# Kernel tuning notes

Measured on AMD Instinct MI355X. Metric: run time of the kernel, lower is better.

## Reference

```python
import jax, jax.numpy as jnp
import numpy as np
from jax import lax

N, L, E, ED, H = 100000, 48, 1600000, 17, 48

def _lin_init(k, fan_in, fan_out):
    kw, kb = jax.random.split(k)
    s = 1.0 / np.sqrt(fan_in)
    W = jax.random.uniform(kw, (fan_in, fan_out), minval=-s, maxval=s, dtype=jnp.float32)
    b = jax.random.uniform(kb, (fan_out,), minval=-s, maxval=s, dtype=jnp.float32)
    return W, b

def setup_inputs() -> dict:
    key = jax.random.key(0)
    ks = jax.random.split(key, 10)
    nodes = jax.random.normal(ks[0], (N, L, 1), dtype=jnp.float32)
    edge_index = jax.random.randint(ks[1], (2, E), 0, N, dtype=jnp.int64) if jax.config.jax_enable_x64 else jax.random.randint(ks[1], (2, E), 0, N, dtype=jnp.int32)
    edge_attr = jax.random.normal(ks[2], (E, ED), dtype=jnp.float32)
    valid = (jax.random.uniform(ks[3], (1, N, L)) < 0.8).astype(jnp.float32)
    r = jnp.zeros((1,), jnp.float32)
    fx = jnp.zeros((1,), jnp.float32)
    W1, b1 = _lin_init(ks[4], ED, H)   # lin_edge[0]
    W2, b2 = _lin_init(ks[5], H, H)    # lin_edge[2]
    Wg, bg = _lin_init(ks[6], H, H)    # gru[0]
    Ww, bw = _lin_init(ks[7], H, 1)    # weight_mlp
    Wf, bf = _lin_init(ks[8], 3, 1)    # fuse_mlp
    return {"nodes": nodes, "edge_index": edge_index, "edge_attr": edge_attr,
            "valid": valid, "r": r, "fx": fx,
            "W1": W1, "b1": b1, "W2": W2, "b2": b2, "Wg": Wg, "bg": bg,
            "Ww": Ww, "bw": bw, "Wf": Wf, "bf": bf}

def _gelu(x):
    return jax.nn.gelu(x, approximate=False)  # torch GELU default is exact erf

def reference(nodes, edge_index, edge_attr, valid, r, fx,
              W1, b1, W2, b2, Wg, bg, Ww, bw, Wf, bf):
    n = nodes.shape[0]
    # torch.no_grad block: mask nodes by valid, flatten (C==1)
    v = lax.stop_gradient(valid[0][..., None])            # [N, L, 1]
    x = lax.stop_gradient((nodes * v).reshape(n, L))      # [N, L]
    original = x
    nv_mask = (1.0 - v).reshape(n, L)                     # not_valid mask [N, L]
    src, dst = edge_index[0], edge_index[1]
    for _ in range(3):
        # lin_edge: 17 -> 48 -> GELU -> 48 -> ReLU  (per edge)
        eh = jax.nn.relu(_gelu(edge_attr @ W1 + b1) @ W2 + b2)      # [E, 48]
        xc = jnp.concatenate([x, v[..., 0]], axis=-1)               # [N, 2L]
        x_j = xc[src]                                               # gather [E, 2L]
        g = _gelu(eh @ Wg + bg)                                     # gru
        w = g @ Ww + bw                                             # [E, 1]
        w = jnp.mean(x_j[:, L:], axis=-1, keepdims=True) * w
        msg = x_j * jax.nn.sigmoid(w)                               # [E, 2L]
        agg = jax.ops.segment_sum(msg, dst, num_segments=n)         # scatter-add [N, 2L]
        new_half = agg[:, :L]                                       # [N, L]
        nn3 = jnp.stack([new_half, x, nv_mask], axis=-1)            # [N, L, 3]
        mask = jax.nn.sigmoid((nn3 @ Wf + bf)[..., 0])              # [N, L]
        x = (1.0 - mask) * x + nv_mask * mask * new_half
        v = jnp.logical_or((original != x)[..., None], v > 0).astype(jnp.float32)
        v = v.at[:, 0].set(0.0)
        nv_mask = (1.0 - v).reshape(n, L)
    return x[0][None]  # [1, L]
```

## Files before the change

kernel.cpp:

```cpp
#include <hip/hip_runtime.h>
#include <math.h>

#define NN 100000
#define LF 48
#define NE 1600000
#define EDIMS 17
#define MASKW 3125
#define CAP_E 16384
#define MAXLOC 12288
#define EB 1563
#define ACT1_CAP 8192
#define ACT2_CAP 64

static_assert(NN == MASKW * 32, "mask width");
static_assert(NE % 4 == 0, "int4 edge scan");

__device__ __forceinline__ float gelu_f(float x) {
    return 0.5f * x * (1.0f + erff(x * 0.7071067811865475f));
}
__device__ __forceinline__ float sigm_f(float x) {
    return 1.0f / (1.0f + expf(-x));
}
__device__ __forceinline__ float wave_sum(float v) {
    #pragma unroll
    for (int off = 32; off > 0; off >>= 1) v += __shfl_down(v, off, 64);
    return __shfl(v, 0, 64);
}

__global__ void expand1_kernel(const int* __restrict__ src, const int* __restrict__ dst,
                               unsigned* __restrict__ M2, unsigned* __restrict__ M1,
                               unsigned* __restrict__ M0, float4* __restrict__ aggz,
                               int4* __restrict__ list0, int* __restrict__ counter)
{
    int tid = blockIdx.x * 256 + threadIdx.x;
    int nthr = (int)gridDim.x * 256;
    for (int i = tid; i < MASKW; i += nthr) { M1[i] = 0u; M0[i] = 0u; }
    for (int i = tid; i < (2 * MAXLOC * LF) / 4; i += nthr)
        aggz[i] = make_float4(0.f, 0.f, 0.f, 0.f);
    if (tid == 0) atomicOr(&M2[0], 1u);
    int e0 = tid * 4;
    if (e0 + 3 < NE) {
        int4 d4 = *(const int4*)(dst + e0);
        int dv[4] = { d4.x, d4.y, d4.z, d4.w };
        #pragma unroll
        for (int k = 0; k < 4; ++k) {
            if (dv[k] == 0) {
                int e = e0 + k;
                int s = src[e];
                int idx = atomicAdd(counter, 1);
                if (idx < CAP_E) list0[idx] = make_int4(s, 0, e, 0);
                atomicOr(&M2[s >> 5], 1u << (s & 31));
            }
        }
    }
}

__global__ void expand2_kernel(const int* __restrict__ src, const int* __restrict__ dst,
                               const unsigned* __restrict__ Min, unsigned* __restrict__ Mout,
                               int4* __restrict__ list, int* __restrict__ counter)
{
    int tid = blockIdx.x * 256 + threadIdx.x;
    int nthr = (int)gridDim.x * 256;
    for (int i = tid; i < MASKW; i += nthr) {
        unsigned m = Min[i];
        if (m) atomicOr(&Mout[i], m);
    }
    int e0 = tid * 4;
    if (e0 + 3 < NE) {
        int4 d4 = *(const int4*)(dst + e0);
        int dv[4] = { d4.x, d4.y, d4.z, d4.w };
        #pragma unroll
        for (int k = 0; k < 4; ++k) {
            int d = dv[k];
            if (Min[d >> 5] & (1u << (d & 31))) {
                int e = e0 + k;
                int s = src[e];
                int idx = atomicAdd(counter, 1);
                if (idx < CAP_E) list[idx] = make_int4(s, d, e, 0);
                atomicOr(&Mout[s >> 5], 1u << (s & 31));
            }
        }
    }
}

__global__ void expand3_kernel(const int* __restrict__ src, const int* __restrict__ dst,
                               const unsigned* __restrict__ M1, unsigned* __restrict__ M0,
                               int4* __restrict__ list, int* __restrict__ counter,
                               int* __restrict__ n2l, int* __restrict__ l2n,
                               int* __restrict__ nloc)
{
    int tid = blockIdx.x * 256 + threadIdx.x;
    int nthr = (int)gridDim.x * 256;
    for (int w = tid; w < MASKW; w += nthr) {
        unsigned bits = M1[w];
        while (bits) {
            int b = __ffs(bits) - 1;
            bits &= bits - 1;
            int node = w * 32 + b;
            int loc = atomicAdd(nloc, 1);
            if (loc < MAXLOC) { n2l[node] = loc; l2n[loc] = node; }
        }
    }
    int e0 = tid * 4;
    if (e0 + 3 < NE) {
        int4 d4 = *(const int4*)(dst + e0);
        int dv[4] = { d4.x, d4.y, d4.z, d4.w };
        #pragma unroll
        for (int k = 0; k < 4; ++k) {
            int d = dv[k];
            if (M1[d >> 5] & (1u << (d & 31))) {
                int e = e0 + k;
                int s = src[e];
                int idx = atomicAdd(counter, 1);
                if (idx < CAP_E) list[idx] = make_int4(s, d, e, 0);
                unsigned sb = 1u << (s & 31);
                unsigned old = atomicOr(&M0[s >> 5], sb);
                if (!(old & sb) && !(M1[s >> 5] & sb)) {
                    int loc = atomicAdd(nloc, 1);
                    if (loc < MAXLOC) { n2l[s] = loc; l2n[loc] = s; }
                }
            }
        }
    }
}

__device__ float w0_compute(long e, const float* __restrict__ ea_g,
                            const float* __restrict__ W1, const float* __restrict__ b1,
                            const float* __restrict__ W2, const float* __restrict__ b2,
                            const float* __restrict__ Wg, const float* __restrict__ bg,
                            const float* __restrict__ Ww, const float* __restrict__ bw,
                            int lane)
{
    float ea = 0.f;
    if (lane < EDIMS) ea = ea_g[e * EDIMS + lane];
    float h1 = 0.f;
    if (lane < 48) {
        float acc = b1[lane];
        #pragma unroll
        for (int k = 0; k < EDIMS; ++k) acc += __shfl(ea, k, 64) * W1[k * 48 + lane];
        h1 = gelu_f(acc);
    }
    float h2 = 0.f;
    if (lane < 48) {
        float acc = b2[lane];
        #pragma unroll 8
        for (int k = 0; k < 48; ++k) acc += __shfl(h1, k, 64) * W2[k * 48 + lane];
        h2 = fmaxf(acc, 0.f);
    }
    float part = 0.f;
    if (lane < 48) {
        float acc = bg[lane];
        #pragma unroll 8
        for (int k = 0; k < 48; ++k) acc += __shfl(h2, k, 64) * Wg[k * 48 + lane];
        part = gelu_f(acc) * Ww[lane];
    }
    return wave_sum(part) + bw[0];
}

__global__ void fused_kernel(const int* __restrict__ counters, const int* __restrict__ l2n,
                             const int* __restrict__ n2l, const unsigned* __restrict__ M1,
                             const float* __restrict__ nodes, const float* __restrict__ valid,
                             float* __restrict__ X0, float* __restrict__ VA,
                             int4* __restrict__ lists, const float* __restrict__ ea_g,
                             const float* __restrict__ W1, const float* __restrict__ b1,
                             const float* __restrict__ W2, const float* __restrict__ b2,
                             const float* __restrict__ Wg, const float* __restrict__ bg,
                             const float* __restrict__ Ww, const float* __restrict__ bw,
                             float* __restrict__ agg0)
{
    int tid = blockIdx.x * 256 + threadIdx.x;
    int nthr = (int)gridDim.x * 256;
    int nl = counters[3]; if (nl > MAXLOC) nl = MAXLOC;
    for (int loc = tid; loc < nl; loc += nthr) {
        int node = l2n[loc];
        if (!(M1[node >> 5] & (1u << (node & 31)))) continue;
        const float4* nv = (const float4*)(valid + (size_t)node * LF);
        const float4* nx = (const float4*)(nodes + (size_t)node * LF);
        float4* X0v = (float4*)(X0 + (size_t)loc * LF);
        float4* V0v = (float4*)(VA + (size_t)loc * LF);
        #pragma unroll
        for (int k = 0; k < 12; ++k) {
            float4 v = nv[k], x = nx[k];
            x.x *= v.x; x.y *= v.y; x.z *= v.z; x.w *= v.w;
            X0v[k] = x; V0v[k] = v;
        }
    }
    int c0 = counters[0]; c0 = (c0 > CAP_E) ? CAP_E : c0;
    int c1 = counters[1]; c1 = (c1 > CAP_E) ? CAP_E : c1;
    int c2 = counters[2]; c2 = (c2 > CAP_E) ? CAP_E : c2;
    int total = c0 + c1 + c2;
    int lane = tid & 63;
    for (int g = tid >> 6; g < total; g += (nthr >> 6)) {
        int4* entp;
        bool isE1 = false;
        if (g < c0)           entp = lists + g;
        else if (g < c0 + c1) entp = lists + CAP_E + (g - c0);
        else                { entp = lists + 2 * CAP_E + (g - c0 - c1); isE1 = true; }
        int4 ent = *entp;
        float w0 = w0_compute((long)ent.z, ea_g, W1, b1, W2, b2, Wg, bg, Ww, bw, lane);
        if (isE1) {
            int s = ent.x;
            int dl = n2l[ent.y]; if ((unsigned)dl >= MAXLOC) dl = 0;
            float v = 0.f, x = 0.f;
            if (lane < 48) {
                v = valid[(size_t)s * LF + lane];
                x = nodes[(size_t)s * LF + lane] * v;
            }
            float mv = wave_sum(v) * (1.0f / 48.0f);
            float sg = sigm_f(mv * w0);
            if (lane < 48) atomicAdd(&agg0[dl * LF + lane], sg * x);
        } else if (lane == 0) {
            int sl = n2l[ent.x]; if ((unsigned)sl >= MAXLOC) sl = 0;
            int dl = n2l[ent.y]; if ((unsigned)dl >= MAXLOC) dl = 0;
            *entp = make_int4(sl, dl, ent.z, __float_as_int(w0));
        }
    }
}

__global__ void __launch_bounds__(1024) tail_kernel(
    const int* __restrict__ counters, const int* __restrict__ l2n, const int* __restrict__ n2l,
    const unsigned* __restrict__ M1, const unsigned* __restrict__ M2,
    const int4* __restrict__ lists, const float* __restrict__ X0,
    float* __restrict__ XA, float* __restrict__ XB,
    float* __restrict__ VA, float* __restrict__ VB,
    float* __restrict__ MVA, float* __restrict__ MVB,
    const float* __restrict__ agg0, float* __restrict__ agg1b,
    const float* __restrict__ Wf, const float* __restrict__ bf, float* __restrict__ out)
{
    __shared__ int act1[ACT1_CAP];
    __shared__ int act2[ACT2_CAP];
    __shared__ int cnts[2];
    __shared__ float agg3s[LF];
    int tid = threadIdx.x;
    if (tid < 2) cnts[tid] = 0;
    if (tid < LF) agg3s[tid] = 0.f;
    __syncthreads();

    int nl = counters[3]; if (nl > MAXLOC) nl = MAXLOC;
    for (int loc = tid; loc < nl; loc += 1024) {
        int node = l2n[loc];
        unsigned bit = 1u << (node & 31);
        unsigned w1 = M1[node >> 5], w2 = M2[node >> 5];
        if (w1 & bit) { int i = atomicAdd(&cnts[0], 1); if (i < ACT1_CAP) act1[i] = loc; }
        if (w2 & bit) { int i = atomicAdd(&cnts[1], 1); if (i < ACT2_CAP) act2[i] = loc; }
    }
    __syncthreads();
    int c1n = cnts[0]; if (c1n > ACT1_CAP) c1n = ACT1_CAP;
    int c2n = cnts[1]; if (c2n > ACT2_CAP) c2n = ACT2_CAP;
    int wave = tid >> 6, lane = tid & 63;
    float wf0 = Wf[0], wf1 = Wf[1], wf2 = Wf[2], bfs = bf[0];

    for (int i = wave; i < c1n; i += 16) {
        int loc = act1[i];
        float nh = 0.f, xo = 0.f, vp = 0.f;
        if (lane < 48) {
            nh = agg0[loc * LF + lane];
            xo = X0[loc * LF + lane];
            vp = VA[loc * LF + lane];
        }
        float nv = 1.0f - vp;
        float m = sigm_f(nh * wf0 + xo * wf1 + nv * wf2 + bfs);
        float xn = (1.0f - m) * xo + nv * m * nh;
        float vn = ((xo != xn) || (vp > 0.f)) ? 1.0f : 0.0f;
        if (lane == 0) vn = 0.0f;
        if (lane < 48) { XA[loc * LF + lane] = xn; VB[loc * LF + lane] = vn; }
        float s = (lane < 48) ? vn : 0.f;
        #pragma unroll
        for (int off = 32; off > 0; off >>= 1) s += __shfl_down(s, off, 64);
        if (lane == 0) MVB[loc] = s * (1.0f / 48.0f);
    }
    __syncthreads();

    int cE2 = counters[1]; if (cE2 > CAP_E) cE2 = CAP_E;
    for (int i = wave; i < cE2; i += 16) {
        int4 ent = lists[CAP_E + i];
        if ((unsigned)ent.x >= MAXLOC || (unsigned)ent.y >= MAXLOC) continue;
        float sg = sigm_f(MVB[ent.x] * __int_as_float(ent.w));
        if (lane < 48) atomicAdd(&agg1b[ent.y * LF + lane], sg * XA[ent.x * LF + lane]);
    }
    __syncthreads();

    for (int i = wave; i < c2n; i += 16) {
        int loc = act2[i];
        float nh = 0.f, xo = 0.f, vp = 0.f, xorig = 0.f;
        if (lane < 48) {
            nh = agg1b[loc * LF + lane];
            xo = XA[loc * LF + lane];
            vp = VB[loc * LF + lane];
            xorig = X0[loc * LF + lane];
        }
        float nv = 1.0f - vp;
        float m = sigm_f(nh * wf0 + xo * wf1 + nv * wf2 + bfs);
        float xn = (1.0f - m) * xo + nv * m * nh;
        float vn = ((xorig != xn) || (vp > 0.f)) ? 1.0f : 0.0f;
        if (lane == 0) vn = 0.0f;
        if (lane < 48) { XB[loc * LF + lane] = xn; VA[loc * LF + lane] = vn; }
        float s = (lane < 48) ? vn : 0.f;
        #pragma unroll
        for (int off = 32; off > 0; off >>= 1) s += __shfl_down(s, off, 64);
        if (lane == 0) MVA[loc] = s * (1.0f / 48.0f);
    }
    __syncthreads();

    int cE3 = counters[0]; if (cE3 > CAP_E) cE3 = CAP_E;
    for (int i = wave; i < cE3; i += 16) {
        int4 ent = lists[i];
        if ((unsigned)ent.x >= MAXLOC) continue;
        float sg = sigm_f(MVA[ent.x] * __int_as_float(ent.w));
        if (lane < 48) atomicAdd(&agg3s[lane], sg * XB[ent.x * LF + lane]);
    }
    __syncthreads();

    if (tid < 48) {
        int loc0 = n2l[0]; if ((unsigned)loc0 >= MAXLOC) loc0 = 0;
        float nh = agg3s[tid];
        float xo = XB[loc0 * LF + tid];
        float vp = VA[loc0 * LF + tid];
        float nv = 1.0f - vp;
        float m = sigm_f(nh * wf0 + xo * wf1 + nv * wf2 + bfs);
        out[tid] = (1.0f - m) * xo + nv * m * nh;
    }
}

extern "C" void kernel_launch(void* const* d_in, const int* in_sizes, int n_in,
                              void* d_out, int out_size, void* d_ws, size_t ws_size,
                              hipStream_t stream)
{
    (void)in_sizes; (void)n_in; (void)out_size;
    const float* nodes = (const float*)d_in[0];
    const int*   eidx  = (const int*)d_in[1];
    const float* eattr = (const float*)d_in[2];
    const float* valid = (const float*)d_in[3];
    const float* W1 = (const float*)d_in[6];
    const float* b1 = (const float*)d_in[7];
    const float* W2 = (const float*)d_in[8];
    const float* b2 = (const float*)d_in[9];
    const float* Wg = (const float*)d_in[10];
    const float* bg = (const float*)d_in[11];
    const float* Ww = (const float*)d_in[12];
    const float* bw = (const float*)d_in[13];
    const float* Wf = (const float*)d_in[14];
    const float* bf = (const float*)d_in[15];
    const int* src = eidx;
    const int* dst = eidx + NE;

    char* ws = (char*)d_ws;
    size_t off = 0;
    auto alloc = [&](size_t bytes) -> char* {
        char* p = ws + off;
        off += (bytes + 255) & ~(size_t)255;
        return p;
    };
    char*     zb = alloc(256 + MASKW * 4);
    int*      counters = (int*)zb;
    unsigned* M2 = (unsigned*)(zb + 256);
    unsigned* M1 = (unsigned*)alloc(MASKW * 4);
    unsigned* M0 = (unsigned*)alloc(MASKW * 4);
    int*      n2l = (int*)alloc((size_t)NN * 4);
    int*      l2n = (int*)alloc((size_t)MAXLOC * 4);
    int4*     lists = (int4*)alloc((size_t)3 * CAP_E * 16);
    float*    X0 = (float*)alloc((size_t)MAXLOC * LF * 4);
    float*    XA = (float*)alloc((size_t)MAXLOC * LF * 4);
    float*    XB = (float*)alloc((size_t)MAXLOC * LF * 4);
    float*    VA = (float*)alloc((size_t)MAXLOC * LF * 4);
    float*    VB = (float*)alloc((size_t)MAXLOC * LF * 4);
    float*    MVA = (float*)alloc((size_t)MAXLOC * 4);
    float*    MVB = (float*)alloc((size_t)MAXLOC * 4);
    float*    agg = (float*)alloc((size_t)2 * MAXLOC * LF * 4);
    if (off > ws_size) return;
    float* agg0  = agg;
    float* agg1b = agg + MAXLOC * LF;

    hipMemsetAsync(zb, 0, 256 + MASKW * 4, stream);

    expand1_kernel<<<EB, 256, 0, stream>>>(src, dst, M2, M1, M0, (float4*)agg,
                                           lists + 0 * CAP_E, counters + 0);
    expand2_kernel<<<EB, 256, 0, stream>>>(src, dst, M2, M1, lists + 1 * CAP_E, counters + 1);
    expand3_kernel<<<EB, 256, 0, stream>>>(src, dst, M1, M0, lists + 2 * CAP_E, counters + 2,
                                           n2l, l2n, counters + 3);
    fused_kernel<<<1024, 256, 0, stream>>>(counters, l2n, n2l, M1, nodes, valid,
                                           X0, VA, lists, eattr,
                                           W1, b1, W2, b2, Wg, bg, Ww, bw, agg0);
    tail_kernel<<<1, 1024, 0, stream>>>(counters, l2n, n2l, M1, M2, lists, X0,
                                        XA, XB, VA, VB, MVA, MVB,
                                        agg0, agg1b, Wf, bf, (float*)d_out);
}
```

Measured before the change: 341.5 us.

## Replace three full edge scans with bucketed CSR build and single-block BFS

Instead of scanning all 1.6M edges three times to expand the 3-hop receptive field of node 0, one pass buckets edge ids by destination (capped at DEG_CAP per node), then a single 1024-thread block walks the frontier with a shared-memory mask. Local indices are assigned in BFS order, which lets the tail kernel drop its active-node compaction and treat node 0 as local index 0. The cost is an atomic-heavy scatter over all edges plus a large bucket array, and the degree and frontier caps can silently drop edges if they are exceeded.

```diff
diff --git a/kernel.cpp b/kernel.cpp
--- a/kernel.cpp
+++ b/kernel.cpp
@@ -8,9 +8,8 @@
 #define MASKW 3125
 #define CAP_E 16384
 #define MAXLOC 12288
-#define EB 1563
-#define ACT1_CAP 8192
-#define ACT2_CAP 64
+#define DEG_CAP 96
+#define SLCAP 4096
 
 static_assert(NN == MASKW * 32, "mask width");
 static_assert(NE % 4 == 0, "int4 edge scan");
@@ -27,100 +26,100 @@
     return __shfl(v, 0, 64);
 }
 
-__global__ void expand1_kernel(const int* __restrict__ src, const int* __restrict__ dst,
-                               unsigned* __restrict__ M2, unsigned* __restrict__ M1,
-                               unsigned* __restrict__ M0, float4* __restrict__ aggz,
-                               int4* __restrict__ list0, int* __restrict__ counter)
+__global__ void scatter_kernel(const int* __restrict__ dst, int* __restrict__ cnt,
+                               int* __restrict__ bkt, float4* __restrict__ aggz)
 {
     int tid = blockIdx.x * 256 + threadIdx.x;
     int nthr = (int)gridDim.x * 256;
-    for (int i = tid; i < MASKW; i += nthr) { M1[i] = 0u; M0[i] = 0u; }
     for (int i = tid; i < (2 * MAXLOC * LF) / 4; i += nthr)
         aggz[i] = make_float4(0.f, 0.f, 0.f, 0.f);
-    if (tid == 0) atomicOr(&M2[0], 1u);
-    int e0 = tid * 4;
-    if (e0 + 3 < NE) {
+    long e0 = (long)tid * 4;
+    if (e0 < NE) {
         int4 d4 = *(const int4*)(dst + e0);
         int dv[4] = { d4.x, d4.y, d4.z, d4.w };
         #pragma unroll
         for (int k = 0; k < 4; ++k) {
-            if (dv[k] == 0) {
-                int e = e0 + k;
-                int s = src[e];
-                int idx = atomicAdd(counter, 1);
-                if (idx < CAP_E) list0[idx] = make_int4(s, 0, e, 0);
-                atomicOr(&M2[s >> 5], 1u << (s & 31));
+            int d = dv[k];
+            int pos = atomicAdd(&cnt[d], 1);
+            if (pos < DEG_CAP) bkt[d * DEG_CAP + pos] = (int)e0 + k;
+        }
+    }
+}
+
+__global__ void __launch_bounds__(1024) bfs_kernel(
+    const int* __restrict__ src, const int* __restrict__ cnt, const int* __restrict__ bkt,
+    int4* __restrict__ lists, int* __restrict__ counters,
+    int* __restrict__ n2l, int* __restrict__ l2n)
+{
+    __shared__ unsigned msk[MASKW];
+    __shared__ int ls[SLCAP];
+    __shared__ int sn[8];
+    int t = threadIdx.x;
+    for (int i = t; i < MASKW; i += 1024) msk[i] = 0u;
+    if (t < 8) sn[t] = 0;
+    __syncthreads();
+    if (t == 0) { ls[0] = 0; msk[0] = 1u; sn[0] = 1; }
+    __syncthreads();
+
+    int c0r = cnt[0]; if (c0r > DEG_CAP) c0r = DEG_CAP;
+    for (int i = t; i < c0r; i += 1024) {
+        int e = bkt[i];
+        int s = src[e];
+        int idx = atomicAdd(&sn[1], 1);
+        if (idx < CAP_E) lists[idx] = make_int4(s, 0, e, 0);
+        unsigned b = 1u << (s & 31);
+        unsigned old = atomicOr(&msk[s >> 5], b);
+        if (!(old & b)) { int j = atomicAdd(&sn[0], 1); if (j < SLCAP) ls[j] = s; }
+    }
+    __syncthreads();
+    int nS2 = sn[0]; if (nS2 > SLCAP) nS2 = SLCAP;
+    __syncthreads();
+
+    for (int j = t; j < nS2 * DEG_CAP; j += 1024) {
+        int i = j / DEG_CAP, slot = j % DEG_CAP;
+        int u = ls[i];
+        int cu = cnt[u]; if (cu > DEG_CAP) cu = DEG_CAP;
+        if (slot < cu) {
+            int e = bkt[u * DEG_CAP + slot];
+            int s = src[e];
+            int idx = atomicAdd(&sn[2], 1);
+            if (idx < CAP_E) lists[CAP_E + idx] = make_int4(s, u, e, 0);
+            unsigned b = 1u << (s & 31);
+            unsigned old = atomicOr(&msk[s >> 5], b);
+            if (!(old & b)) { int jj = atomicAdd(&sn[0], 1); if (jj < SLCAP) ls[jj] = s; }
+        }
+    }
+    __syncthreads();
+    int nS1 = sn[0]; if (nS1 > SLCAP) nS1 = SLCAP;
+    for (int i = t; i < nS1; i += 1024) { int u = ls[i]; n2l[u] = i; l2n[i] = u; }
+    if (t == 0) sn[4] = nS1;
+    __syncthreads();
+
+    for (int j = t; j < nS1 * DEG_CAP; j += 1024) {
+        int i = j / DEG_CAP, slot = j % DEG_CAP;
+        int u = ls[i];
+        int cu = cnt[u]; if (cu > DEG_CAP) cu = DEG_CAP;
+        if (slot < cu) {
+            int e = bkt[u * DEG_CAP + slot];
+            int s = src[e];
+            int idx = atomicAdd(&sn[3], 1);
+            if (idx < CAP_E) lists[2 * CAP_E + idx] = make_int4(s, u, e, 0);
+            unsigned b = 1u << (s & 31);
+            unsigned old = atomicOr(&msk[s >> 5], b);
+            if (!(old & b)) {
+                int loc = atomicAdd(&sn[4], 1);
+                if (loc < MAXLOC) { n2l[s] = loc; l2n[loc] = s; }
             }
         }
     }
-}
-
-__global__ void expand2_kernel(const int* __restrict__ src, const int* __restrict__ dst,
-                               const unsigned* __restrict__ Min, unsigned* __restrict__ Mout,
-                               int4* __restrict__ list, int* __restrict__ counter)
-{
-    int tid = blockIdx.x * 256 + threadIdx.x;
-    int nthr = (int)gridDim.x * 256;
-    for (int i = tid; i < MASKW; i += nthr) {
-        unsigned m = Min[i];
-        if (m) atomicOr(&Mout[i], m);
-    }
-    int e0 = tid * 4;
-    if (e0 + 3 < NE) {
-        int4 d4 = *(const int4*)(dst + e0);
-        int dv[4] = { d4.x, d4.y, d4.z, d4.w };
-        #pragma unroll
-        for (int k = 0; k < 4; ++k) {
-            int d = dv[k];
-            if (Min[d >> 5] & (1u << (d & 31))) {
-                int e = e0 + k;
-                int s = src[e];
-                int idx = atomicAdd(counter, 1);
-                if (idx < CAP_E) list[idx] = make_int4(s, d, e, 0);
-                atomicOr(&Mout[s >> 5], 1u << (s & 31));
-            }
-        }
-    }
-}
-
-__global__ void expand3_kernel(const int* __restrict__ src, const int* __restrict__ dst,
-                               const unsigned* __restrict__ M1, unsigned* __restrict__ M0,
-                               int4* __restrict__ list, int* __restrict__ counter,
-                               int* __restrict__ n2l, int* __restrict__ l2n,
-                               int* __restrict__ nloc)
-{
-    int tid = blockIdx.x * 256 + threadIdx.x;
-    int nthr = (int)gridDim.x * 256;
-    for (int w = tid; w < MASKW; w += nthr) {
-        unsigned bits = M1[w];
-        while (bits) {
-            int b = __ffs(bits) - 1;
-            bits &= bits - 1;
-            int node = w * 32 + b;
-            int loc = atomicAdd(nloc, 1);
-            if (loc < MAXLOC) { n2l[node] = loc; l2n[loc] = node; }
-        }
-    }
-    int e0 = tid * 4;
-    if (e0 + 3 < NE) {
-        int4 d4 = *(const int4*)(dst + e0);
-        int dv[4] = { d4.x, d4.y, d4.z, d4.w };
-        #pragma unroll
-        for (int k = 0; k < 4; ++k) {
-            int d = dv[k];
-            if (M1[d >> 5] & (1u << (d & 31))) {
-                int e = e0 + k;
-                int s = src[e];
-                int idx = atomicAdd(counter, 1);
-                if (idx < CAP_E) list[idx] = make_int4(s, d, e, 0);
-                unsigned sb = 1u << (s & 31);
-                unsigned old = atomicOr(&M0[s >> 5], sb);
-                if (!(old & sb) && !(M1[s >> 5] & sb)) {
-                    int loc = atomicAdd(nloc, 1);
-                    if (loc < MAXLOC) { n2l[s] = loc; l2n[loc] = s; }
-                }
-            }
-        }
+    __syncthreads();
+    if (t == 0) {
+        int a = sn[1]; counters[0] = (a > CAP_E) ? CAP_E : a;
+        a = sn[2];     counters[1] = (a > CAP_E) ? CAP_E : a;
+        a = sn[3];     counters[2] = (a > CAP_E) ? CAP_E : a;
+        a = sn[4];     counters[3] = (a > MAXLOC) ? MAXLOC : a;
+        counters[4] = nS1;
+        counters[5] = nS2;
     }
 }
 
@@ -158,7 +157,7 @@
 }
 
 __global__ void fused_kernel(const int* __restrict__ counters, const int* __restrict__ l2n,
-                             const int* __restrict__ n2l, const unsigned* __restrict__ M1,
+                             const int* __restrict__ n2l,
                              const float* __restrict__ nodes, const float* __restrict__ valid,
                              float* __restrict__ X0, float* __restrict__ VA,
                              int4* __restrict__ lists, const float* __restrict__ ea_g,
@@ -170,10 +169,9 @@
 {
     int tid = blockIdx.x * 256 + threadIdx.x;
     int nthr = (int)gridDim.x * 256;
-    int nl = counters[3]; if (nl > MAXLOC) nl = MAXLOC;
-    for (int loc = tid; loc < nl; loc += nthr) {
+    int nS1 = counters[4]; if (nS1 > MAXLOC) nS1 = MAXLOC;
+    for (int loc = tid; loc < nS1; loc += nthr) {
         int node = l2n[loc];
-        if (!(M1[node >> 5] & (1u << (node & 31)))) continue;
         const float4* nv = (const float4*)(valid + (size_t)node * LF);
         const float4* nx = (const float4*)(nodes + (size_t)node * LF);
         float4* X0v = (float4*)(X0 + (size_t)loc * LF);
@@ -218,8 +216,7 @@
 }
 
 __global__ void __launch_bounds__(1024) tail_kernel(
-    const int* __restrict__ counters, const int* __restrict__ l2n, const int* __restrict__ n2l,
-    const unsigned* __restrict__ M1, const unsigned* __restrict__ M2,
+    const int* __restrict__ counters,
     const int4* __restrict__ lists, const float* __restrict__ X0,
     float* __restrict__ XA, float* __restrict__ XB,
     float* __restrict__ VA, float* __restrict__ VB,
@@ -227,31 +224,17 @@
     const float* __restrict__ agg0, float* __restrict__ agg1b,
     const float* __restrict__ Wf, const float* __restrict__ bf, float* __restrict__ out)
 {
-    __shared__ int act1[ACT1_CAP];
-    __shared__ int act2[ACT2_CAP];
-    __shared__ int cnts[2];
     __shared__ float agg3s[LF];
     int tid = threadIdx.x;
-    if (tid < 2) cnts[tid] = 0;
     if (tid < LF) agg3s[tid] = 0.f;
     __syncthreads();
 
-    int nl = counters[3]; if (nl > MAXLOC) nl = MAXLOC;
-    for (int loc = tid; loc < nl; loc += 1024) {
-        int node = l2n[loc];
-        unsigned bit = 1u << (node & 31);
-        unsigned w1 = M1[node >> 5], w2 = M2[node >> 5];
-        if (w1 & bit) { int i = atomicAdd(&cnts[0], 1); if (i < ACT1_CAP) act1[i] = loc; }
-        if (w2 & bit) { int i = atomicAdd(&cnts[1], 1); if (i < ACT2_CAP) act2[i] = loc; }
-    }
-    __syncthreads();
-    int c1n = cnts[0]; if (c1n > ACT1_CAP) c1n = ACT1_CAP;
-    int c2n = cnts[1]; if (c2n > ACT2_CAP) c2n = ACT2_CAP;
+    int c1n = counters[4]; if (c1n > MAXLOC) c1n = MAXLOC;
+    int c2n = counters[5]; if (c2n > MAXLOC) c2n = MAXLOC;
     int wave = tid >> 6, lane = tid & 63;
     float wf0 = Wf[0], wf1 = Wf[1], wf2 = Wf[2], bfs = bf[0];
 
-    for (int i = wave; i < c1n; i += 16) {
-        int loc = act1[i];
+    for (int loc = wave; loc < c1n; loc += 16) {
         float nh = 0.f, xo = 0.f, vp = 0.f;
         if (lane < 48) {
             nh = agg0[loc * LF + lane];
@@ -280,8 +263,7 @@
     }
     __syncthreads();
 
-    for (int i = wave; i < c2n; i += 16) {
-        int loc = act2[i];
+    for (int loc = wave; loc < c2n; loc += 16) {
         float nh = 0.f, xo = 0.f, vp = 0.f, xorig = 0.f;
         if (lane < 48) {
             nh = agg1b[loc * LF + lane];
@@ -312,10 +294,9 @@
     __syncthreads();
 
     if (tid < 48) {
-        int loc0 = n2l[0]; if ((unsigned)loc0 >= MAXLOC) loc0 = 0;
         float nh = agg3s[tid];
-        float xo = XB[loc0 * LF + tid];
-        float vp = VA[loc0 * LF + tid];
+        float xo = XB[tid];
+        float vp = VA[tid];
         float nv = 1.0f - vp;
         float m = sigm_f(nh * wf0 + xo * wf1 + nv * wf2 + bfs);
         out[tid] = (1.0f - m) * xo + nv * m * nh;
@@ -351,11 +332,10 @@
         off += (bytes + 255) & ~(size_t)255;
         return p;
     };
-    char*     zb = alloc(256 + MASKW * 4);
+    char*     zb = alloc(256 + (size_t)NN * 4);
     int*      counters = (int*)zb;
-    unsigned* M2 = (unsigned*)(zb + 256);
-    unsigned* M1 = (unsigned*)alloc(MASKW * 4);
-    unsigned* M0 = (unsigned*)alloc(MASKW * 4);
+    int*      cnt = (int*)(zb + 256);
+    int*      bkt = (int*)alloc((size_t)NN * DEG_CAP * 4);
     int*      n2l = (int*)alloc((size_t)NN * 4);
     int*      l2n = (int*)alloc((size_t)MAXLOC * 4);
     int4*     lists = (int4*)alloc((size_t)3 * CAP_E * 16);
@@ -371,17 +351,14 @@
     float* agg0  = agg;
     float* agg1b = agg + MAXLOC * LF;
 
-    hipMemsetAsync(zb, 0, 256 + MASKW * 4, stream);
-
-    expand1_kernel<<<EB, 256, 0, stream>>>(src, dst, M2, M1, M0, (float4*)agg,
-                                           lists + 0 * CAP_E, counters + 0);
-    expand2_kernel<<<EB, 256, 0, stream>>>(src, dst, M2, M1, lists + 1 * CAP_E, counters + 1);
-    expand3_kernel<<<EB, 256, 0, stream>>>(src, dst, M1, M0, lists + 2 * CAP_E, counters + 2,
-                                           n2l, l2n, counters + 3);
-    fused_kernel<<<1024, 256, 0, stream>>>(counters, l2n, n2l, M1, nodes, valid,
+    hipMemsetAsync(zb, 0, 256 + (size_t)NN * 4, stream);
+
+    scatter_kernel<<<NE / 4 / 256, 256, 0, stream>>>(dst, cnt, bkt, (float4*)agg);
+    bfs_kernel<<<1, 1024, 0, stream>>>(src, cnt, bkt, lists, counters, n2l, l2n);
+    fused_kernel<<<1024, 256, 0, stream>>>(counters, l2n, n2l, nodes, valid,
                                            X0, VA, lists, eattr,
                                            W1, b1, W2, b2, Wg, bg, Ww, bw, agg0);
-    tail_kernel<<<1, 1024, 0, stream>>>(counters, l2n, n2l, M1, M2, lists, X0,
+    tail_kernel<<<1, 1024, 0, stream>>>(counters, lists, X0,
                                         XA, XB, VA, VB, MVA, MVB,
                                         agg0, agg1b, Wf, bf, (float*)d_out);
 }
```

Result: slower. 405.8 us (+18.8%).
